# Optimization experiments

Hardware: AMD Instinct MI355X
Metric: run time of the kernel (lower is better)

Reference implementation:

```python
import jax, jax.numpy as jnp
import numpy as np

E = 16        # num_experts
TOPK = 2      # num_experts_per_tok


def setup_inputs() -> dict:
    key = jax.random.key(0)
    ks = jax.random.split(key, 8)
    B, S, H, I, IS = 4, 2048, 1024, 512, 2048
    std = 0.02
    return {
        "hidden_states": jax.random.normal(ks[0], (B, S, H), jnp.float32),
        "gate_w": jax.random.normal(ks[1], (E, H), jnp.float32) * std,
        "gate_up_proj": jax.random.normal(ks[2], (E, 2 * I, H), jnp.float32) * std,
        "down_proj": jax.random.normal(ks[3], (E, H, I), jnp.float32) * std,
        "shared_gate_proj": jax.random.normal(ks[4], (IS, H), jnp.float32) * std,
        "shared_up_proj": jax.random.normal(ks[5], (IS, H), jnp.float32) * std,
        "shared_down_proj": jax.random.normal(ks[6], (H, IS), jnp.float32) * std,
        "shared_expert_gate_w": jax.random.normal(ks[7], (1, H), jnp.float32) * std,
    }


def _moe(x, gate_w, gate_up_proj, down_proj, sgp, sup, sdp, segw):
    # x: [N, H] flattened tokens
    N = x.shape[0]
    router_logits = x @ gate_w.T                      # [N, E]
    probs = jax.nn.softmax(router_logits, axis=-1)
    routing_weights, selected = jax.lax.top_k(probs, TOPK)   # [N, TOPK]
    routing_weights = routing_weights / routing_weights.sum(-1, keepdims=True)
    # combine weights scattered into dense [N, E] (per-token per-expert gate)
    combine = jnp.zeros((N, E), x.dtype).at[jnp.arange(N)[:, None], selected].add(routing_weights)

    def body(acc, ws):
        gu_w, d_w, cw = ws                            # [2I,H], [H,I], [N]
        gu = x @ gu_w.T                               # [N, 2I]
        g, u = jnp.split(gu, 2, axis=-1)
        h = jax.nn.silu(g) * u                        # [N, I]
        return acc + cw[:, None] * (h @ d_w.T), None

    expert_out, _ = jax.lax.scan(body, jnp.zeros_like(x), (gate_up_proj, down_proj, combine.T))

    # shared expert with sigmoid token gate
    shared_h = jax.nn.silu(x @ sgp.T) * (x @ sup.T)   # [N, IS]
    shared_out = (shared_h @ sdp.T) * jax.nn.sigmoid(x @ segw.T)  # [N, H]
    out = expert_out + shared_out

    # aux (load-balancing) loss
    counts = jnp.sum(jax.nn.one_hot(selected, E, dtype=x.dtype), axis=(0, 1))  # [E]
    frac_tokens = counts / (N * TOPK)
    frac_probs = probs.sum(0) / N
    aux_loss = E * jnp.sum(frac_tokens * frac_probs)
    return out, aux_loss


def reference(hidden_states, gate_w, gate_up_proj, down_proj, shared_gate_proj, shared_up_proj, shared_down_proj, shared_expert_gate_w):
    B, S, H = hidden_states.shape
    out, aux = _moe(hidden_states.reshape(-1, H), gate_w, gate_up_proj, down_proj,
                    shared_gate_proj, shared_up_proj, shared_down_proj, shared_expert_gate_w)
    return out.reshape(B, S, H), aux
```

## Files before the change

kernel.cpp:

```cpp
#include <hip/hip_runtime.h>
#include <hip/hip_bf16.h>
#include <stdint.h>


#define N_TOK 8192
#define HDIM 1024
#define NEXP 16
#define IEXP 512
#define ISH 2048

typedef __bf16 bf16x8 __attribute__((ext_vector_type(8)));
typedef float f32x4 __attribute__((ext_vector_type(4)));

#define OFF_XBF   ((size_t)0)
#define OFF_WSG   ((size_t)16777216)
#define OFF_WSU   ((size_t)20971520)
#define OFF_WSD   ((size_t)25165824)
#define OFF_SH    ((size_t)29360128)
#define OFF_HEXP  ((size_t)62914560)
#define OFF_IDS   ((size_t)79691776)
#define OFF_TW    ((size_t)80216064)
#define OFF_META  ((size_t)80740352)
#define OFF_SIG   ((size_t)80740608)
#define OFF_LG    ((size_t)80773376)

static __device__ __forceinline__ unsigned short f2bf(float f) {
  unsigned int u = __float_as_uint(f);
  u += 0x7fffu + ((u >> 16) & 1u);
  return (unsigned short)(u >> 16);
}
static __device__ __forceinline__ int pack_bf2(float a, float b) {
  return (int)f2bf(a) | ((int)f2bf(b) << 16);
}
static __device__ __forceinline__ void gl_lds16(const void* g, void* l) {
  __builtin_amdgcn_global_load_lds(
      (const __attribute__((address_space(1))) unsigned int*)g,
      (__attribute__((address_space(3))) unsigned int*)l, 16, 0, 0);
}

__global__ void cvt_kernel(const float* __restrict__ src,
                           unsigned short* __restrict__ dst, int n4) {
  int i = blockIdx.x * 256 + threadIdx.x;
  if (i >= n4) return;
  float4 v = ((const float4*)src)[i];
  uint2 o;
  o.x = (unsigned)pack_bf2(v.x, v.y);
  o.y = (unsigned)pack_bf2(v.z, v.w);
  ((uint2*)dst)[i] = o;
}

__global__ __launch_bounds__(256) void logits_kernel(
    const float* __restrict__ X, const float* __restrict__ GW,
    const float* __restrict__ SEGW, float* __restrict__ LG) {
  int wid = threadIdx.x >> 6, lane = threadIdx.x & 63;
  int tok = blockIdx.x * 4 + wid;
  const float* xr = X + (size_t)tok * HDIM;
  float xv[16];
#pragma unroll
  for (int i = 0; i < 16; i++) xv[i] = xr[lane + 64 * i];
  float myv = 0.f;
#pragma unroll
  for (int e = 0; e < 17; e++) {
    const float* wr = (e < 16) ? (GW + (size_t)e * HDIM) : SEGW;
    float p = 0.f;
#pragma unroll
    for (int i = 0; i < 16; i++) p += xv[i] * wr[lane + 64 * i];
#pragma unroll
    for (int off = 32; off >= 1; off >>= 1) p += __shfl_xor(p, off, 64);
    if (lane == e) myv = p;
  }
  if (lane < 17) LG[(size_t)tok * 32 + lane] = myv;
}

__global__ __launch_bounds__(256) void route_kernel(
    const float* __restrict__ LG, int* __restrict__ cnt,
    float* __restrict__ pps, int* __restrict__ ids,
    float* __restrict__ tw, float* __restrict__ sig) {
  __shared__ int lcnt[16];
  __shared__ int lbase[16];
  __shared__ float lps[16];
  int tid = threadIdx.x;
  int tok = blockIdx.x * 256 + tid;
  if (tid < 16) { lcnt[tid] = 0; lps[tid] = 0.f; }
  __syncthreads();
  const float4* row = (const float4*)(LG + (size_t)tok * 32);
  float4 v0 = row[0], v1 = row[1], v2 = row[2], v3 = row[3];
  float g16 = row[4].x;
  float lg[16] = {v0.x, v0.y, v0.z, v0.w, v1.x, v1.y, v1.z, v1.w,
                  v2.x, v2.y, v2.z, v2.w, v3.x, v3.y, v3.z, v3.w};
  float mx = lg[0];
#pragma unroll
  for (int e = 1; e < 16; e++) mx = fmaxf(mx, lg[e]);
  float pr[16], s = 0.f;
#pragma unroll
  for (int e = 0; e < 16; e++) { pr[e] = __expf(lg[e] - mx); s += pr[e]; }
  float inv_s = 1.f / s;
  float p1 = -1.f, p2 = -1.f; int i1 = 0, i2 = 0;
#pragma unroll
  for (int e = 0; e < 16; e++) {
    if (pr[e] > p1) { p2 = p1; i2 = i1; p1 = pr[e]; i1 = e; }
    else if (pr[e] > p2) { p2 = pr[e]; i2 = e; }
  }
  float wsum = p1 + p2;
  int s1 = atomicAdd(&lcnt[i1], 1);
  int s2 = atomicAdd(&lcnt[i2], 1);
#pragma unroll
  for (int e = 0; e < 16; e++) atomicAdd(&lps[e], pr[e] * inv_s);
  sig[tok] = 1.f / (1.f + __expf(-g16));
  __syncthreads();
  if (tid < 16) {
    lbase[tid] = atomicAdd(&cnt[tid], lcnt[tid]);
    atomicAdd(&pps[tid], lps[tid]);
  }
  __syncthreads();
  int d1 = i1 * N_TOK + lbase[i1] + s1;
  int d2 = i2 * N_TOK + lbase[i2] + s2;
  ids[d1] = tok; tw[d1] = p1 / wsum;
  ids[d2] = tok; tw[d2] = p2 / wsum;
}

__global__ void offs_aux_kernel(const int* __restrict__ cnt, int* __restrict__ off,
                                const float* __restrict__ probs_sum,
                                float* __restrict__ out_aux) {
  if (threadIdx.x == 0 && blockIdx.x == 0) {
    int run = 0; float aux = 0.f;
    for (int e = 0; e < NEXP; e++) {
      off[e] = run; run += cnt[e];
      aux += ((float)cnt[e] / (float)(N_TOK * 2)) * (probs_sum[e] / (float)N_TOK);
    }
    off[16] = run;
    *out_aux = (float)NEXP * aux;
  }
}

__global__ __launch_bounds__(256) void shared_gemm1_kernel(
    const unsigned short* __restrict__ X, const unsigned short* __restrict__ Wg,
    const unsigned short* __restrict__ Wu, unsigned short* __restrict__ H) {
  __shared__ __align__(16) unsigned short As[128 * 32];
  __shared__ __align__(16) unsigned short Bs1[64 * 32];
  __shared__ __align__(16) unsigned short Bs2[64 * 32];
  int m0 = blockIdx.y * 128, n0 = blockIdx.x * 64;
  int t = threadIdx.x, lane = t & 63, w = t >> 6;
  int wm = (w & 1) * 64, wn = (w >> 1) * 32;
  int arow = t >> 2, akb = (t & 3) * 8;
  const unsigned short* ap0 = X + (size_t)(m0 + arow) * HDIM + akb;
  const unsigned short* ap1 = X + (size_t)(m0 + 64 + arow) * HDIM + akb;
  const unsigned short* bp1 = Wg + (size_t)(n0 + arow) * HDIM + akb;
  const unsigned short* bp2 = Wu + (size_t)(n0 + arow) * HDIM + akb;
  f32x4 z = {0.f, 0.f, 0.f, 0.f};
  f32x4 accg[4][2], accu[4][2];
#pragma unroll
  for (int i = 0; i < 4; i++)
#pragma unroll
    for (int j = 0; j < 2; j++) { accg[i][j] = z; accu[i][j] = z; }
  for (int k0 = 0; k0 < HDIM; k0 += 32) {
    __syncthreads();
    gl_lds16(ap0 + k0, &As[t * 8]);
    gl_lds16(ap1 + k0, &As[2048 + t * 8]);
    gl_lds16(bp1 + k0, &Bs1[t * 8]);
    gl_lds16(bp2 + k0, &Bs2[t * 8]);
    __syncthreads();
    int fr = lane & 15, fc = (lane >> 4) * 8;
    bf16x8 af[4], bg[2], bu[2];
#pragma unroll
    for (int i = 0; i < 4; i++) af[i] = *(const bf16x8*)&As[(wm + i * 16 + fr) * 32 + fc];
#pragma unroll
    for (int j = 0; j < 2; j++) {
      bg[j] = *(const bf16x8*)&Bs1[(wn + j * 16 + fr) * 32 + fc];
      bu[j] = *(const bf16x8*)&Bs2[(wn + j * 16 + fr) * 32 + fc];
    }
#pragma unroll
    for (int i = 0; i < 4; i++)
#pragma unroll
      for (int j = 0; j < 2; j++) {
        accg[i][j] = __builtin_amdgcn_mfma_f32_16x16x32_bf16(af[i], bg[j], accg[i][j], 0, 0, 0);
        accu[i][j] = __builtin_amdgcn_mfma_f32_16x16x32_bf16(af[i], bu[j], accu[i][j], 0, 0, 0);
      }
  }
  int col = lane & 15, rq = (lane >> 4) * 4;
#pragma unroll
  for (int i = 0; i < 4; i++)
#pragma unroll
    for (int j = 0; j < 2; j++)
#pragma unroll
      for (int r = 0; r < 4; r++) {
        int mm = m0 + wm + i * 16 + rq + r;
        int nn = n0 + wn + j * 16 + col;
        float g = accg[i][j][r], u = accu[i][j][r];
        float h = g / (1.f + __expf(-g)) * u;
        H[(size_t)mm * ISH + nn] = f2bf(h);
      }
}

__global__ __launch_bounds__(256) void shared_gemm2_kernel(
    const unsigned short* __restrict__ H, const unsigned short* __restrict__ Wd,
    const float* __restrict__ sig, float* __restrict__ Out) {
  __shared__ __align__(16) unsigned short As[128 * 32];
  __shared__ __align__(16) unsigned short Bs[128 * 32];
  int m0 = blockIdx.y * 128, n0 = blockIdx.x * 128;
  int t = threadIdx.x, lane = t & 63, w = t >> 6;
  int wm = (w & 1) * 64, wn = (w >> 1) * 64;
  int arow = t >> 2, akb = (t & 3) * 8;
  const unsigned short* apA0 = H + (size_t)(m0 + arow) * ISH + akb;
  const unsigned short* apA1 = H + (size_t)(m0 + 64 + arow) * ISH + akb;
  const unsigned short* apB0 = Wd + (size_t)(n0 + arow) * ISH + akb;
  const unsigned short* apB1 = Wd + (size_t)(n0 + 64 + arow) * ISH + akb;
  f32x4 z = {0.f, 0.f, 0.f, 0.f};
  f32x4 acc[4][4];
#pragma unroll
  for (int i = 0; i < 4; i++)
#pragma unroll
    for (int j = 0; j < 4; j++) acc[i][j] = z;
  for (int k0 = 0; k0 < ISH; k0 += 32) {
    __syncthreads();
    gl_lds16(apA0 + k0, &As[t * 8]);
    gl_lds16(apA1 + k0, &As[2048 + t * 8]);
    gl_lds16(apB0 + k0, &Bs[t * 8]);
    gl_lds16(apB1 + k0, &Bs[2048 + t * 8]);
    __syncthreads();
    int fr = lane & 15, fc = (lane >> 4) * 8;
    bf16x8 af[4], bfr[4];
#pragma unroll
    for (int i = 0; i < 4; i++) {
      af[i] = *(const bf16x8*)&As[(wm + i * 16 + fr) * 32 + fc];
      bfr[i] = *(const bf16x8*)&Bs[(wn + i * 16 + fr) * 32 + fc];
    }
#pragma unroll
    for (int i = 0; i < 4; i++)
#pragma unroll
      for (int j = 0; j < 4; j++)
        acc[i][j] = __builtin_amdgcn_mfma_f32_16x16x32_bf16(af[i], bfr[j], acc[i][j], 0, 0, 0);
  }
  int col = lane & 15, rq = (lane >> 4) * 4;
#pragma unroll
  for (int i = 0; i < 4; i++)
#pragma unroll
    for (int r = 0; r < 4; r++) {
      int mm = m0 + wm + i * 16 + rq + r;
      float sg = sig[mm];
#pragma unroll
      for (int j = 0; j < 4; j++) {
        int nn = n0 + wn + j * 16 + col;
        Out[(size_t)mm * HDIM + nn] = acc[i][j][r] * sg;
      }
    }
}

__global__ __launch_bounds__(256) void exp_gemm1_kernel(
    const unsigned short* __restrict__ X, const unsigned short* __restrict__ WGUb,
    const int* __restrict__ ids, const int* __restrict__ cnt,
    const int* __restrict__ off, unsigned short* __restrict__ Hexp) {
  int e = blockIdx.z;
  int ne = cnt[e];
  int m0 = blockIdx.y * 128;
  if (m0 >= ne) return;
  __shared__ __align__(16) unsigned short As[128 * 32];
  __shared__ __align__(16) unsigned short Bs1[64 * 32];
  __shared__ __align__(16) unsigned short Bs2[64 * 32];
  int n0 = blockIdx.x * 64;
  const int* eids = ids + e * N_TOK;
  int base = off[e];
  int t = threadIdx.x, lane = t & 63, w = t >> 6;
  int wm = (w & 1) * 64, wn = (w >> 1) * 32;
  int arow = t >> 2, akb = (t & 3) * 8;
  int s0 = m0 + arow, s1 = m0 + 64 + arow;
  int t0 = (s0 < ne) ? eids[s0] : 0;
  int t1 = (s1 < ne) ? eids[s1] : 0;
  const unsigned short* ap0 = X + (size_t)t0 * HDIM + akb;
  const unsigned short* ap1 = X + (size_t)t1 * HDIM + akb;
  const unsigned short* bpg = WGUb + ((size_t)e * 1024 + n0 + arow) * HDIM + akb;
  const unsigned short* bpu = WGUb + ((size_t)e * 1024 + 512 + n0 + arow) * HDIM + akb;
  f32x4 z = {0.f, 0.f, 0.f, 0.f};
  f32x4 accg[4][2], accu[4][2];
#pragma unroll
  for (int i = 0; i < 4; i++)
#pragma unroll
    for (int j = 0; j < 2; j++) { accg[i][j] = z; accu[i][j] = z; }
  for (int k0 = 0; k0 < HDIM; k0 += 32) {
    __syncthreads();
    gl_lds16(ap0 + k0, &As[t * 8]);
    gl_lds16(ap1 + k0, &As[2048 + t * 8]);
    gl_lds16(bpg + k0, &Bs1[t * 8]);
    gl_lds16(bpu + k0, &Bs2[t * 8]);
    __syncthreads();
    int fr = lane & 15, fc = (lane >> 4) * 8;
    bf16x8 af[4], bg[2], bu[2];
#pragma unroll
    for (int i = 0; i < 4; i++) af[i] = *(const bf16x8*)&As[(wm + i * 16 + fr) * 32 + fc];
#pragma unroll
    for (int j = 0; j < 2; j++) {
      bg[j] = *(const bf16x8*)&Bs1[(wn + j * 16 + fr) * 32 + fc];
      bu[j] = *(const bf16x8*)&Bs2[(wn + j * 16 + fr) * 32 + fc];
    }
#pragma unroll
    for (int i = 0; i < 4; i++)
#pragma unroll
      for (int j = 0; j < 2; j++) {
        accg[i][j] = __builtin_amdgcn_mfma_f32_16x16x32_bf16(af[i], bg[j], accg[i][j], 0, 0, 0);
        accu[i][j] = __builtin_amdgcn_mfma_f32_16x16x32_bf16(af[i], bu[j], accu[i][j], 0, 0, 0);
      }
  }
  int col = lane & 15, rq = (lane >> 4) * 4;
#pragma unroll
  for (int i = 0; i < 4; i++)
#pragma unroll
    for (int j = 0; j < 2; j++)
#pragma unroll
      for (int r = 0; r < 4; r++) {
        int slot = m0 + wm + i * 16 + rq + r;
        if (slot < ne) {
          int nn = n0 + wn + j * 16 + col;
          float g = accg[i][j][r], u = accu[i][j][r];
          float h = g / (1.f + __expf(-g)) * u;
          Hexp[(size_t)(base + slot) * IEXP + nn] = f2bf(h);
        }
      }
}

__global__ __launch_bounds__(256) void exp_gemm2_kernel(
    const unsigned short* __restrict__ Hexp, const unsigned short* __restrict__ WDb,
    const int* __restrict__ ids, const float* __restrict__ tw,
    const int* __restrict__ cnt, const int* __restrict__ off,
    float* __restrict__ Out) {
  int e = blockIdx.z;
  int ne = cnt[e];
  int m0 = blockIdx.y * 128;
  if (m0 >= ne) return;
  __shared__ __align__(16) unsigned short As[128 * 32];
  __shared__ __align__(16) unsigned short Bs[128 * 32];
  int n0 = blockIdx.x * 128;
  const int* eids = ids + e * N_TOK;
  const float* etw = tw + e * N_TOK;
  int base = off[e];
  int t = threadIdx.x, lane = t & 63, w = t >> 6;
  int wm = (w & 1) * 64, wn = (w >> 1) * 64;
  int arow = t >> 2, akb = (t & 3) * 8;
  int ra0 = base + m0 + arow;        if (ra0 > 16383) ra0 = 16383;
  int ra1 = base + m0 + 64 + arow;   if (ra1 > 16383) ra1 = 16383;
  const unsigned short* ap0 = Hexp + (size_t)ra0 * IEXP + akb;
  const unsigned short* ap1 = Hexp + (size_t)ra1 * IEXP + akb;
  const unsigned short* bp0 = WDb + ((size_t)e * HDIM + n0 + arow) * IEXP + akb;
  const unsigned short* bp1 = WDb + ((size_t)e * HDIM + n0 + 64 + arow) * IEXP + akb;
  f32x4 z = {0.f, 0.f, 0.f, 0.f};
  f32x4 acc[4][4];
#pragma unroll
  for (int i = 0; i < 4; i++)
#pragma unroll
    for (int j = 0; j < 4; j++) acc[i][j] = z;
  for (int k0 = 0; k0 < IEXP; k0 += 32) {
    __syncthreads();
    gl_lds16(ap0 + k0, &As[t * 8]);
    gl_lds16(ap1 + k0, &As[2048 + t * 8]);
    gl_lds16(bp0 + k0, &Bs[t * 8]);
    gl_lds16(bp1 + k0, &Bs[2048 + t * 8]);
    __syncthreads();
    int fr = lane & 15, fc = (lane >> 4) * 8;
    bf16x8 af[4], bfr[4];
#pragma unroll
    for (int i = 0; i < 4; i++) {
      af[i] = *(const bf16x8*)&As[(wm + i * 16 + fr) * 32 + fc];
      bfr[i] = *(const bf16x8*)&Bs[(wn + i * 16 + fr) * 32 + fc];
    }
#pragma unroll
    for (int i = 0; i < 4; i++)
#pragma unroll
      for (int j = 0; j < 4; j++)
        acc[i][j] = __builtin_amdgcn_mfma_f32_16x16x32_bf16(af[i], bfr[j], acc[i][j], 0, 0, 0);
  }
  int col = lane & 15, rq = (lane >> 4) * 4;
#pragma unroll
  for (int i = 0; i < 4; i++)
#pragma unroll
    for (int r = 0; r < 4; r++) {
      int slot = m0 + wm + i * 16 + rq + r;
      if (slot < ne) {
        int tok = eids[slot];
        float wgt = etw[slot];
#pragma unroll
        for (int j = 0; j < 4; j++) {
          int nn = n0 + wn + j * 16 + col;
          atomicAdd(&Out[(size_t)tok * HDIM + nn], acc[i][j][r] * wgt);
        }
      }
    }
}

extern "C" void kernel_launch(void* const* d_in, const int* in_sizes, int n_in,
                              void* d_out, int out_size, void* d_ws, size_t ws_size,
                              hipStream_t stream) {
  const float* X   = (const float*)d_in[0];
  const float* GW  = (const float*)d_in[1];
  const float* WGU = (const float*)d_in[2];
  const float* WDN = (const float*)d_in[3];
  const float* WSG = (const float*)d_in[4];
  const float* WSU = (const float*)d_in[5];
  const float* WSD = (const float*)d_in[6];
  const float* SEGW = (const float*)d_in[7];
  float* Out = (float*)d_out;
  char* ws = (char*)d_ws;

  unsigned short* xbf  = (unsigned short*)(ws + OFF_XBF);
  unsigned short* wsg  = (unsigned short*)(ws + OFF_WSG);
  unsigned short* wsu  = (unsigned short*)(ws + OFF_WSU);
  unsigned short* wsd  = (unsigned short*)(ws + OFF_WSD);
  unsigned short* sh   = (unsigned short*)(ws + OFF_SH);
  unsigned short* hexp = (unsigned short*)(ws + OFF_HEXP);
  int*   ids  = (int*)(ws + OFF_IDS);
  float* tw   = (float*)(ws + OFF_TW);
  int*   cnt  = (int*)(ws + OFF_META);
  int*   off  = (int*)(ws + OFF_META + 64);
  float* pps  = (float*)(ws + OFF_META + 144);
  float* sig  = (float*)(ws + OFF_SIG);
  float* lg   = (float*)(ws + OFF_LG);
  unsigned short* wgu_bf = (unsigned short*)(ws + OFF_SH);
  unsigned short* wdn_bf = (unsigned short*)(ws + OFF_XBF);

  hipMemsetAsync(ws + OFF_META, 0, 256, stream);

  {
    int n4;
    n4 = (N_TOK * HDIM) / 4;
    cvt_kernel<<<(n4 + 255) / 256, 256, 0, stream>>>(X, xbf, n4);
    n4 = (ISH * HDIM) / 4;
    cvt_kernel<<<(n4 + 255) / 256, 256, 0, stream>>>(WSG, wsg, n4);
    cvt_kernel<<<(n4 + 255) / 256, 256, 0, stream>>>(WSU, wsu, n4);
    n4 = (HDIM * ISH) / 4;
    cvt_kernel<<<(n4 + 255) / 256, 256, 0, stream>>>(WSD, wsd, n4);
  }

  logits_kernel<<<N_TOK / 4, 256, 0, stream>>>(X, GW, SEGW, lg);
  route_kernel<<<N_TOK / 256, 256, 0, stream>>>(lg, cnt, pps, ids, tw, sig);
  offs_aux_kernel<<<1, 64, 0, stream>>>(cnt, off, pps, Out + (size_t)N_TOK * HDIM);

  shared_gemm1_kernel<<<dim3(ISH / 64, N_TOK / 128), 256, 0, stream>>>(xbf, wsg, wsu, sh);
  shared_gemm2_kernel<<<dim3(HDIM / 128, N_TOK / 128), 256, 0, stream>>>(sh, wsd, sig, Out);

  {
    int n4 = (NEXP * 2 * IEXP * HDIM) / 4;
    cvt_kernel<<<(n4 + 255) / 256, 256, 0, stream>>>(WGU, wgu_bf, n4);
  }
  exp_gemm1_kernel<<<dim3(IEXP / 64, N_TOK / 128, NEXP), 256, 0, stream>>>(
      xbf, wgu_bf, ids, cnt, off, hexp);
  {
    int n4 = (NEXP * HDIM * IEXP) / 4;
    cvt_kernel<<<(n4 + 255) / 256, 256, 0, stream>>>(WDN, wdn_bf, n4);
  }
  exp_gemm2_kernel<<<dim3(HDIM / 128, N_TOK / 128, NEXP), 256, 0, stream>>>(
      hexp, wdn_bf, ids, tw, cnt, off, Out);
}
```

Measured before the change: 528.0 us.

## Replace atomic scatter in expert down-proj with bf16 buffer and gather combine

The expert down-projection kernel now writes its per-slot results as bf16 into a contiguous buffer instead of atomically adding weighted floats into the output. A new combine kernel reads each token's two expert rows via stored slot indices and weights and adds them into the output. The x-to-bf16 conversion is also folded into the logits kernel, which drops one pass over x. The aim is to remove heavy atomic contention at the cost of an extra write/read pass and bf16 rounding of expert outputs.

Measured after the change: 491.5 us. 1.07x faster.

```diff
diff --git a/kernel.cpp b/kernel.cpp
--- a/kernel.cpp
+++ b/kernel.cpp
@@ -19,10 +19,11 @@
 #define OFF_SH    ((size_t)29360128)
 #define OFF_HEXP  ((size_t)62914560)
 #define OFF_IDS   ((size_t)79691776)
-#define OFF_TW    ((size_t)80216064)
-#define OFF_META  ((size_t)80740352)
-#define OFF_SIG   ((size_t)80740608)
-#define OFF_LG    ((size_t)80773376)
+#define OFF_META  ((size_t)80216064)
+#define OFF_SIG   ((size_t)80216320)
+#define OFF_LG    ((size_t)80249088)
+#define OFF_SLOT  ((size_t)81297664)
+#define OFF_TWAB  ((size_t)81363200)
 
 static __device__ __forceinline__ unsigned short f2bf(float f) {
   unsigned int u = __float_as_uint(f);
@@ -31,6 +32,9 @@
 }
 static __device__ __forceinline__ int pack_bf2(float a, float b) {
   return (int)f2bf(a) | ((int)f2bf(b) << 16);
+}
+static __device__ __forceinline__ float bf2f(unsigned short u) {
+  return __uint_as_float(((unsigned int)u) << 16);
 }
 static __device__ __forceinline__ void gl_lds16(const void* g, void* l) {
   __builtin_amdgcn_global_load_lds(
@@ -51,13 +55,17 @@
 
 __global__ __launch_bounds__(256) void logits_kernel(
     const float* __restrict__ X, const float* __restrict__ GW,
-    const float* __restrict__ SEGW, float* __restrict__ LG) {
+    const float* __restrict__ SEGW, float* __restrict__ LG,
+    unsigned short* __restrict__ XBF) {
   int wid = threadIdx.x >> 6, lane = threadIdx.x & 63;
   int tok = blockIdx.x * 4 + wid;
   const float* xr = X + (size_t)tok * HDIM;
+  unsigned short* xw = XBF + (size_t)tok * HDIM;
   float xv[16];
 #pragma unroll
   for (int i = 0; i < 16; i++) xv[i] = xr[lane + 64 * i];
+#pragma unroll
+  for (int i = 0; i < 16; i++) xw[lane + 64 * i] = f2bf(xv[i]);
   float myv = 0.f;
 #pragma unroll
   for (int e = 0; e < 17; e++) {
@@ -75,7 +83,8 @@
 __global__ __launch_bounds__(256) void route_kernel(
     const float* __restrict__ LG, int* __restrict__ cnt,
     float* __restrict__ pps, int* __restrict__ ids,
-    float* __restrict__ tw, float* __restrict__ sig) {
+    int* __restrict__ slotAB, float* __restrict__ twAB,
+    float* __restrict__ sig) {
   __shared__ int lcnt[16];
   __shared__ int lbase[16];
   __shared__ float lps[16];
@@ -113,10 +122,13 @@
     atomicAdd(&pps[tid], lps[tid]);
   }
   __syncthreads();
-  int d1 = i1 * N_TOK + lbase[i1] + s1;
-  int d2 = i2 * N_TOK + lbase[i2] + s2;
-  ids[d1] = tok; tw[d1] = p1 / wsum;
-  ids[d2] = tok; tw[d2] = p2 / wsum;
+  int sl1 = lbase[i1] + s1, sl2 = lbase[i2] + s2;
+  ids[i1 * N_TOK + sl1] = tok;
+  ids[i2 * N_TOK + sl2] = tok;
+  slotAB[tok * 2]     = (i1 << 14) | sl1;
+  slotAB[tok * 2 + 1] = (i2 << 14) | sl2;
+  twAB[tok * 2]     = p1 / wsum;
+  twAB[tok * 2 + 1] = p2 / wsum;
 }
 
 __global__ void offs_aux_kernel(const int* __restrict__ cnt, int* __restrict__ off,
@@ -319,9 +331,8 @@
 
 __global__ __launch_bounds__(256) void exp_gemm2_kernel(
     const unsigned short* __restrict__ Hexp, const unsigned short* __restrict__ WDb,
-    const int* __restrict__ ids, const float* __restrict__ tw,
     const int* __restrict__ cnt, const int* __restrict__ off,
-    float* __restrict__ Out) {
+    unsigned short* __restrict__ Eout) {
   int e = blockIdx.z;
   int ne = cnt[e];
   int m0 = blockIdx.y * 128;
@@ -329,8 +340,6 @@
   __shared__ __align__(16) unsigned short As[128 * 32];
   __shared__ __align__(16) unsigned short Bs[128 * 32];
   int n0 = blockIdx.x * 128;
-  const int* eids = ids + e * N_TOK;
-  const float* etw = tw + e * N_TOK;
   int base = off[e];
   int t = threadIdx.x, lane = t & 63, w = t >> 6;
   int wm = (w & 1) * 64, wn = (w >> 1) * 64;
@@ -374,15 +383,33 @@
     for (int r = 0; r < 4; r++) {
       int slot = m0 + wm + i * 16 + rq + r;
       if (slot < ne) {
-        int tok = eids[slot];
-        float wgt = etw[slot];
 #pragma unroll
         for (int j = 0; j < 4; j++) {
           int nn = n0 + wn + j * 16 + col;
-          atomicAdd(&Out[(size_t)tok * HDIM + nn], acc[i][j][r] * wgt);
+          Eout[(size_t)(base + slot) * HDIM + nn] = f2bf(acc[i][j][r]);
         }
       }
     }
+}
+
+__global__ __launch_bounds__(256) void combine_kernel(
+    const unsigned short* __restrict__ Eout, const int* __restrict__ slotAB,
+    const float* __restrict__ twAB, const int* __restrict__ off,
+    float* __restrict__ Out) {
+  int tok = blockIdx.x, t = threadIdx.x;
+  int sa = slotAB[tok * 2], sb = slotAB[tok * 2 + 1];
+  float wa = twAB[tok * 2], wb = twAB[tok * 2 + 1];
+  int ra = off[sa >> 14] + (sa & 16383);
+  int rb = off[sb >> 14] + (sb & 16383);
+  const ushort4 a4 = *(const ushort4*)(Eout + (size_t)ra * HDIM + t * 4);
+  const ushort4 b4 = *(const ushort4*)(Eout + (size_t)rb * HDIM + t * 4);
+  float* po = Out + (size_t)tok * HDIM + t * 4;
+  float4 o = *(const float4*)po;
+  o.x += wa * bf2f(a4.x) + wb * bf2f(b4.x);
+  o.y += wa * bf2f(a4.y) + wb * bf2f(b4.y);
+  o.z += wa * bf2f(a4.z) + wb * bf2f(b4.z);
+  o.w += wa * bf2f(a4.w) + wb * bf2f(b4.w);
+  *(float4*)po = o;
 }
 
 extern "C" void kernel_launch(void* const* d_in, const int* in_sizes, int n_in,
@@ -406,21 +433,21 @@
   unsigned short* sh   = (unsigned short*)(ws + OFF_SH);
   unsigned short* hexp = (unsigned short*)(ws + OFF_HEXP);
   int*   ids  = (int*)(ws + OFF_IDS);
-  float* tw   = (float*)(ws + OFF_TW);
   int*   cnt  = (int*)(ws + OFF_META);
   int*   off  = (int*)(ws + OFF_META + 64);
   float* pps  = (float*)(ws + OFF_META + 144);
   float* sig  = (float*)(ws + OFF_SIG);
   float* lg   = (float*)(ws + OFF_LG);
+  int*   slotAB = (int*)(ws + OFF_SLOT);
+  float* twAB   = (float*)(ws + OFF_TWAB);
   unsigned short* wgu_bf = (unsigned short*)(ws + OFF_SH);
   unsigned short* wdn_bf = (unsigned short*)(ws + OFF_XBF);
+  unsigned short* eout   = (unsigned short*)(ws + OFF_SH);
 
   hipMemsetAsync(ws + OFF_META, 0, 256, stream);
 
   {
     int n4;
-    n4 = (N_TOK * HDIM) / 4;
-    cvt_kernel<<<(n4 + 255) / 256, 256, 0, stream>>>(X, xbf, n4);
     n4 = (ISH * HDIM) / 4;
     cvt_kernel<<<(n4 + 255) / 256, 256, 0, stream>>>(WSG, wsg, n4);
     cvt_kernel<<<(n4 + 255) / 256, 256, 0, stream>>>(WSU, wsu, n4);
@@ -428,8 +455,8 @@
     cvt_kernel<<<(n4 + 255) / 256, 256, 0, stream>>>(WSD, wsd, n4);
   }
 
-  logits_kernel<<<N_TOK / 4, 256, 0, stream>>>(X, GW, SEGW, lg);
-  route_kernel<<<N_TOK / 256, 256, 0, stream>>>(lg, cnt, pps, ids, tw, sig);
+  logits_kernel<<<N_TOK / 4, 256, 0, stream>>>(X, GW, SEGW, lg, xbf);
+  route_kernel<<<N_TOK / 256, 256, 0, stream>>>(lg, cnt, pps, ids, slotAB, twAB, sig);
   offs_aux_kernel<<<1, 64, 0, stream>>>(cnt, off, pps, Out + (size_t)N_TOK * HDIM);
 
   shared_gemm1_kernel<<<dim3(ISH / 64, N_TOK / 128), 256, 0, stream>>>(xbf, wsg, wsu, sh);
@@ -446,5 +473,6 @@
     cvt_kernel<<<(n4 + 255) / 256, 256, 0, stream>>>(WDN, wdn_bf, n4);
   }
   exp_gemm2_kernel<<<dim3(HDIM / 128, N_TOK / 128, NEXP), 256, 0, stream>>>(
-      hexp, wdn_bf, ids, tw, cnt, off, Out);
-}
+      hexp, wdn_bf, cnt, off, eout);
+  combine_kernel<<<N_TOK, 256, 0, stream>>>(eout, slotAB, twAB, off, Out);
+}
```
